# Kernel tuning notes

Hardware: AMD Instinct MI355X
Metric: run time of the kernel (lower is better)

## Reference

```python
import jax, jax.numpy as jnp
import numpy as np
from jax import lax

WINDOW_SIZE = 11
SIGMA = 1.5
DATA_RANGE = 1.0
C1 = (0.01 * DATA_RANGE) ** 2
C2 = (0.03 * DATA_RANGE) ** 2


def _gauss_1d():
    half = WINDOW_SIZE // 2
    xs = np.arange(WINDOW_SIZE, dtype=np.float32)
    g = np.exp(-((xs - half) ** 2) / (2.0 * SIGMA ** 2)).astype(np.float32)
    g = g / g.sum()
    return jnp.asarray(g)


def _blur3d(v, g1d):
    """Depthwise 3D Gaussian blur via three separable 1D convs (same math as
    conv3d with the outer-product window, padding=window_size//2)."""
    C = v.shape[1]
    pad = WINDOW_SIZE // 2
    dn = lax.conv_dimension_numbers(v.shape, (C, 1, WINDOW_SIZE, 1, 1),
                                    ('NCDHW', 'OIDHW', 'NCDHW'))
    for axis in range(3):  # D, H, W
        kshape = [1, 1, 1]
        kshape[axis] = WINDOW_SIZE
        kern = jnp.broadcast_to(g1d.reshape(kshape)[None, None], (C, 1, *kshape))
        padding = [(0, 0)] * 3
        padding[axis] = (pad, pad)
        v = lax.conv_general_dilated(v, kern, window_strides=(1, 1, 1),
                                     padding=padding, dimension_numbers=dn,
                                     feature_group_count=C)
    return v


def setup_inputs() -> dict:
    key = jax.random.key(0)
    k1, k2 = jax.random.split(key)
    shape = (2, 1, 160, 160, 160)
    x = jax.random.uniform(k1, shape, dtype=jnp.float32)
    y = jax.random.uniform(k2, shape, dtype=jnp.float32)
    return {"x": x, "y": y}


def reference(x, y):
    g1d = _gauss_1d()
    mu_x = _blur3d(x, g1d)
    mu_y = _blur3d(y, g1d)
    mu_x_sq = mu_x * mu_x
    mu_y_sq = mu_y * mu_y
    mu_xy = mu_x * mu_y
    sigma_x_sq = _blur3d(x * x, g1d) - mu_x_sq
    sigma_y_sq = _blur3d(y * y, g1d) - mu_y_sq
    sigma_xy = _blur3d(x * y, g1d) - mu_xy
    ssim_map = ((2.0 * mu_xy + C1) * (2.0 * sigma_xy + C2)) / (
        (mu_x_sq + mu_y_sq + C1) * (sigma_x_sq + sigma_y_sq + C2))
    return ssim_map.mean()  # size_average=True
```

## Files before the change

kernel.cpp:

```cpp
#include <hip/hip_runtime.h>
#include <cmath>

#define WS  11
#define NX  160
#define NXY (NX*NX)
#define NB  2
#define TH  16
#define TW  32
#define MH  26
#define MST 36
#define DCHUNK 40
#define PLANE_I 8192000

struct GaussW { float g[WS]; };

__global__ __launch_bounds__(256, 5) void k_wh(const float* __restrict__ x,
                                               const float* __restrict__ y,
                                               float* __restrict__ A,
                                               GaussW gw) {
    __shared__ float mid[5][MH][MST];

    const int tid = threadIdx.x;
    const int b  = blockIdx.z / NX;
    const int d  = blockIdx.z % NX;
    const int h0 = blockIdx.y * TH;
    const int w0 = blockIdx.x * TW;
    const int slice = (b * NX + d) * NXY;

    if (tid < 208) {
        const int wr = tid >> 3;
        const int wq = tid & 7;
        const int gh = h0 - 5 + wr;
        const bool rowok = (unsigned)gh < (unsigned)NX;
        const int c0 = w0 + 4 * wq - 8;
        const int rbase = slice + gh * NX;

        float wx[20], wy[20];
        #pragma unroll
        for (int i = 0; i < 5; ++i) {
            const int ci = c0 + 4 * i;
            float4 xv = {0,0,0,0}, yv = {0,0,0,0};
            if (rowok) {
                if (ci >= 0 && ci + 3 < NX) {
                    xv = *(const float4*)(x + rbase + ci);
                    yv = *(const float4*)(y + rbase + ci);
                } else {
                    float ex[4] = {0,0,0,0}, ey[4] = {0,0,0,0};
                    #pragma unroll
                    for (int e = 0; e < 4; ++e)
                        if ((unsigned)(ci + e) < (unsigned)NX) {
                            ex[e] = x[rbase + ci + e];
                            ey[e] = y[rbase + ci + e];
                        }
                    xv = make_float4(ex[0], ex[1], ex[2], ex[3]);
                    yv = make_float4(ey[0], ey[1], ey[2], ey[3]);
                }
            }
            wx[4*i] = xv.x; wx[4*i+1] = xv.y; wx[4*i+2] = xv.z; wx[4*i+3] = xv.w;
            wy[4*i] = yv.x; wy[4*i+1] = yv.y; wy[4*i+2] = yv.z; wy[4*i+3] = yv.w;
        }
        float a0[4] = {0,0,0,0}, a1[4] = {0,0,0,0}, a2[4] = {0,0,0,0},
              a3[4] = {0,0,0,0}, a4[4] = {0,0,0,0};
        #pragma unroll
        for (int k = 0; k < WS; ++k) {
            const float gk = gw.g[k];
            #pragma unroll
            for (int jj = 0; jj < 4; ++jj) {
                const float xv = wx[3 + jj + k];
                const float yv = wy[3 + jj + k];
                const float t0 = gk * xv, t1 = gk * yv;
                a0[jj] += t0;       a1[jj] += t1;
                a2[jj] += t0 * xv;  a3[jj] += t1 * yv;  a4[jj] += t0 * yv;
            }
        }
        *(float4*)&mid[0][wr][4*wq] = make_float4(a0[0], a0[1], a0[2], a0[3]);
        *(float4*)&mid[1][wr][4*wq] = make_float4(a1[0], a1[1], a1[2], a1[3]);
        *(float4*)&mid[2][wr][4*wq] = make_float4(a2[0], a2[1], a2[2], a2[3]);
        *(float4*)&mid[3][wr][4*wq] = make_float4(a3[0], a3[1], a3[2], a3[3]);
        *(float4*)&mid[4][wr][4*wq] = make_float4(a4[0], a4[1], a4[2], a4[3]);
    }
    __syncthreads();

    if (tid < 160) {
        const int hf  = tid >> 5;
        const int hr0 = ((tid >> 3) & 3) << 2;
        const int hq4 = (tid & 7) << 2;
        float4 o0 = {0,0,0,0}, o1 = {0,0,0,0}, o2 = {0,0,0,0}, o3 = {0,0,0,0};
        #pragma unroll
        for (int k2 = 0; k2 < 14; ++k2) {
            const float4 v = *(const float4*)&mid[hf][hr0 + k2][hq4];
            if (k2 <= 10) { const float g = gw.g[k2];
                o0.x += g*v.x; o0.y += g*v.y; o0.z += g*v.z; o0.w += g*v.w; }
            if (k2 >= 1 && k2 <= 11) { const float g = gw.g[k2-1];
                o1.x += g*v.x; o1.y += g*v.y; o1.z += g*v.z; o1.w += g*v.w; }
            if (k2 >= 2 && k2 <= 12) { const float g = gw.g[k2-2];
                o2.x += g*v.x; o2.y += g*v.y; o2.z += g*v.z; o2.w += g*v.w; }
            if (k2 >= 3) { const float g = gw.g[k2-3];
                o3.x += g*v.x; o3.y += g*v.y; o3.z += g*v.z; o3.w += g*v.w; }
        }
        const int obase = hf * PLANE_I + slice + (h0 + hr0) * NX + w0 + hq4;
        *(float4*)(A + obase)          = o0;
        *(float4*)(A + obase + NX)     = o1;
        *(float4*)(A + obase + 2*NX)   = o2;
        *(float4*)(A + obase + 3*NX)   = o3;
    }
}

__global__ __launch_bounds__(256) void k_d(const float* __restrict__ A,
                                           float* __restrict__ partial,
                                           GaussW gw) {
    const int tid = threadIdx.x;
    const long long gidx = (long long)blockIdx.x * 256 + tid;
    const int NCOL = NB * NX * NX;
    const int chunk = (int)(gidx / NCOL);
    const int col   = (int)(gidx % NCOL);
    const int b  = col / (NX * NX);
    const int hw = col % (NX * NX);
    const int base = b * (NX * NXY) + hw;
    const int d0 = chunk * DCHUNK;

    float win[5][WS];
    #pragma unroll
    for (int i = 0; i < WS; ++i) {
        const int di = d0 - 5 + i;
        const bool ok = (di >= 0 && di < NX);
        const int o = base + (ok ? di : 0) * NXY;
        #pragma unroll
        for (int f = 0; f < 5; ++f)
            win[f][i] = ok ? A[f * PLANE_I + o] : 0.f;
    }

    float acc = 0.f;
    for (int dd = 0; dd < DCHUNK; ++dd) {
        float m[5];
        #pragma unroll
        for (int f = 0; f < 5; ++f) {
            float s = 0.f;
            #pragma unroll
            for (int i = 0; i < WS; ++i) s += gw.g[i] * win[f][i];
            m[f] = s;
        }
        const float mux = m[0], muy = m[1];
        const float mux2 = mux * mux, muy2 = muy * muy, muxy = mux * muy;
        const float sxx = m[2] - mux2, syy = m[3] - muy2, sxy = m[4] - muxy;
        const float num = (2.f * muxy + 1.0e-4f) * (2.f * sxy + 9.0e-4f);
        const float den = (mux2 + muy2 + 1.0e-4f) * (sxx + syy + 9.0e-4f);
        acc += num / den;

        const int dn = d0 + dd + 6;
        const bool ok = (dn < NX);
        const int o = base + (ok ? dn : 0) * NXY;
        #pragma unroll
        for (int f = 0; f < 5; ++f) {
            #pragma unroll
            for (int i = 0; i < WS - 1; ++i) win[f][i] = win[f][i + 1];
            win[f][WS - 1] = ok ? A[f * PLANE_I + o] : 0.f;
        }
    }

    for (int off = 32; off > 0; off >>= 1) acc += __shfl_down(acc, off, 64);
    __shared__ float wsum[4];
    if ((tid & 63) == 0) wsum[tid >> 6] = acc;
    __syncthreads();
    if (tid == 0) partial[blockIdx.x] = wsum[0] + wsum[1] + wsum[2] + wsum[3];
}

__global__ __launch_bounds__(256) void k_red(const float* __restrict__ partial,
                                             int n, float* __restrict__ out) {
    double s = 0.0;
    for (int i = threadIdx.x; i < n; i += 256) s += (double)partial[i];
    __shared__ double sd[256];
    sd[threadIdx.x] = s;
    __syncthreads();
    for (int st = 128; st > 0; st >>= 1) {
        if (threadIdx.x < st) sd[threadIdx.x] += sd[threadIdx.x + st];
        __syncthreads();
    }
    if (threadIdx.x == 0)
        out[0] = (float)(sd[0] / (double)((long long)NB * NX * NXY));
}

extern "C" void kernel_launch(void* const* d_in, const int* in_sizes, int n_in,
                              void* d_out, int out_size, void* d_ws, size_t ws_size,
                              hipStream_t stream) {
    const float* x = (const float*)d_in[0];
    const float* y = (const float*)d_in[1];
    float* A = (float*)d_ws;
    float* partial = (float*)((char*)d_ws + (size_t)5 * PLANE_I * sizeof(float));

    GaussW gw;
    {
        float tmp[WS]; float s = 0.f;
        for (int i = 0; i < WS; ++i) {
            const double e = exp(-(double)((i - 5) * (i - 5)) / 4.5);
            tmp[i] = (float)e; s += tmp[i];
        }
        for (int i = 0; i < WS; ++i) gw.g[i] = tmp[i] / s;
    }

    dim3 g1(NX / TW, NX / TH, NB * NX);
    k_wh<<<g1, 256, 0, stream>>>(x, y, A, gw);

    const int nblk2 = (NB * NX * NX * (NX / DCHUNK)) / 256;
    k_d<<<nblk2, 256, 0, stream>>>(A, partial, gw);

    k_red<<<1, 256, 0, stream>>>(partial, nblk2, (float*)d_out);
}
```

Measured before the change: 116.4 us.

## Double-buffer input slices via async global-to-LDS loads across depth planes per block

The W/H blur kernel now has each block process five consecutive depth slices instead of one. It stages each slice's x and y tile into LDS with global_load_lds while the previous slice is being computed, and clamps addresses so edge zero-padding is applied in registers. The aim is to hide global load latency behind compute and cut per-block launch overhead. In exchange the kernel uses more LDS, lowers the occupancy hint from 5 to 4, and adds extra barriers per slice.

```diff
diff --git a/kernel.cpp b/kernel.cpp
--- a/kernel.cpp
+++ b/kernel.cpp
@@ -9,100 +9,141 @@
 #define TW  32
 #define MH  26
 #define MST 36
+#define SST 48
+#define DPB 5
 #define DCHUNK 40
 #define PLANE_I 8192000
 
 struct GaussW { float g[WS]; };
 
-__global__ __launch_bounds__(256, 5) void k_wh(const float* __restrict__ x,
-                                               const float* __restrict__ y,
-                                               float* __restrict__ A,
-                                               GaussW gw) {
+__device__ __forceinline__ void gload_lds16(const float* g, void* l) {
+    __builtin_amdgcn_global_load_lds(
+        (const __attribute__((address_space(1))) void*)g,
+        (__attribute__((address_space(3))) void*)l, 16, 0, 0);
+}
+
+__global__ __launch_bounds__(256, 4) void k_whp(const float* __restrict__ x,
+                                                const float* __restrict__ y,
+                                                float* __restrict__ A,
+                                                GaussW gw) {
+    __shared__ float sx[2][MH][SST];
+    __shared__ float sy[2][MH][SST];
     __shared__ float mid[5][MH][MST];
 
     const int tid = threadIdx.x;
-    const int b  = blockIdx.z / NX;
-    const int d  = blockIdx.z % NX;
+    const int w0 = blockIdx.x * TW;
     const int h0 = blockIdx.y * TH;
-    const int w0 = blockIdx.x * TW;
-    const int slice = (b * NX + d) * NXY;
-
-    if (tid < 208) {
-        const int wr = tid >> 3;
-        const int wq = tid & 7;
-        const int gh = h0 - 5 + wr;
-        const bool rowok = (unsigned)gh < (unsigned)NX;
-        const int c0 = w0 + 4 * wq - 8;
-        const int rbase = slice + gh * NX;
-
-        float wx[20], wy[20];
-        #pragma unroll
-        for (int i = 0; i < 5; ++i) {
-            const int ci = c0 + 4 * i;
-            float4 xv = {0,0,0,0}, yv = {0,0,0,0};
+    const int b  = blockIdx.z >> 5;
+    const int d0 = (blockIdx.z & 31) * DPB;
+    const int vol = b * (NX * NXY);
+
+    const int r0s = tid / 12, q0s = tid % 12;
+    const int a0g = vol + min(max(h0 - 5 + r0s, 0), NX - 1) * NX
+                        + min(max(w0 - 8 + 4 * q0s, 0), NX - 4);
+    const int ch1 = 256 + tid;
+    const int r1s = ch1 / 12, q1s = ch1 % 12;
+    const int a1g = vol + min(max(h0 - 5 + r1s, 0), NX - 1) * NX
+                        + min(max(w0 - 8 + 4 * q1s, 0), NX - 4);
+    const int wvoff = (tid >> 6) << 10;
+
+    const int wr = tid >> 3;
+    const int wq = tid & 7;
+    const bool wbact = tid < 208;
+    const bool rowok = (unsigned)(h0 - 5 + wr) < (unsigned)NX;
+    const bool edgeblk = (w0 == 0) || (w0 == NX - TW);
+
+    const int hf  = tid >> 5;
+    const int hr0 = ((tid >> 3) & 3) << 2;
+    const int hq4 = (tid & 7) << 2;
+    const bool hbact = tid < 160;
+    const int obase0 = hf * PLANE_I + vol + (h0 + hr0) * NX + w0 + hq4;
+
+    auto stage = [&](int buf, int d) {
+        const int dof = d * NXY;
+        gload_lds16(x + a0g + dof, (char*)&sx[buf][0][0] + wvoff);
+        gload_lds16(y + a0g + dof, (char*)&sy[buf][0][0] + wvoff);
+        if (tid < 56) {
+            gload_lds16(x + a1g + dof, (char*)&sx[buf][0][0] + 4096);
+            gload_lds16(y + a1g + dof, (char*)&sy[buf][0][0] + 4096);
+        }
+    };
+
+    stage(0, d0);
+    __syncthreads();
+
+    int cur = 0;
+    for (int s = 0; s < DPB; ++s) {
+        if (s + 1 < DPB) stage(cur ^ 1, d0 + s + 1);
+
+        if (wbact) {
             if (rowok) {
-                if (ci >= 0 && ci + 3 < NX) {
-                    xv = *(const float4*)(x + rbase + ci);
-                    yv = *(const float4*)(y + rbase + ci);
-                } else {
-                    float ex[4] = {0,0,0,0}, ey[4] = {0,0,0,0};
+                float wx[20], wy[20];
+                #pragma unroll
+                for (int i = 0; i < 5; ++i) {
+                    const float4 xv = *(const float4*)&sx[cur][wr][4 * wq + 4 * i];
+                    const float4 yv = *(const float4*)&sy[cur][wr][4 * wq + 4 * i];
+                    wx[4*i] = xv.x; wx[4*i+1] = xv.y; wx[4*i+2] = xv.z; wx[4*i+3] = xv.w;
+                    wy[4*i] = yv.x; wy[4*i+1] = yv.y; wy[4*i+2] = yv.z; wy[4*i+3] = yv.w;
+                }
+                if (edgeblk) {
                     #pragma unroll
-                    for (int e = 0; e < 4; ++e)
-                        if ((unsigned)(ci + e) < (unsigned)NX) {
-                            ex[e] = x[rbase + ci + e];
-                            ey[e] = y[rbase + ci + e];
+                    for (int m = 0; m < 20; ++m)
+                        if ((unsigned)(w0 - 8 + 4 * wq + m) >= (unsigned)NX) {
+                            wx[m] = 0.f; wy[m] = 0.f;
                         }
-                    xv = make_float4(ex[0], ex[1], ex[2], ex[3]);
-                    yv = make_float4(ey[0], ey[1], ey[2], ey[3]);
                 }
+                float a0[4] = {0,0,0,0}, a1[4] = {0,0,0,0}, a2[4] = {0,0,0,0},
+                      a3[4] = {0,0,0,0}, a4[4] = {0,0,0,0};
+                #pragma unroll
+                for (int k = 0; k < WS; ++k) {
+                    const float gk = gw.g[k];
+                    #pragma unroll
+                    for (int jj = 0; jj < 4; ++jj) {
+                        const float xv = wx[3 + jj + k];
+                        const float yv = wy[3 + jj + k];
+                        const float t0 = gk * xv, t1 = gk * yv;
+                        a0[jj] += t0;       a1[jj] += t1;
+                        a2[jj] += t0 * xv;  a3[jj] += t1 * yv;  a4[jj] += t0 * yv;
+                    }
+                }
+                *(float4*)&mid[0][wr][4*wq] = make_float4(a0[0], a0[1], a0[2], a0[3]);
+                *(float4*)&mid[1][wr][4*wq] = make_float4(a1[0], a1[1], a1[2], a1[3]);
+                *(float4*)&mid[2][wr][4*wq] = make_float4(a2[0], a2[1], a2[2], a2[3]);
+                *(float4*)&mid[3][wr][4*wq] = make_float4(a3[0], a3[1], a3[2], a3[3]);
+                *(float4*)&mid[4][wr][4*wq] = make_float4(a4[0], a4[1], a4[2], a4[3]);
+            } else {
+                const float4 z4 = make_float4(0.f, 0.f, 0.f, 0.f);
+                *(float4*)&mid[0][wr][4*wq] = z4;
+                *(float4*)&mid[1][wr][4*wq] = z4;
+                *(float4*)&mid[2][wr][4*wq] = z4;
+                *(float4*)&mid[3][wr][4*wq] = z4;
+                *(float4*)&mid[4][wr][4*wq] = z4;
             }
-            wx[4*i] = xv.x; wx[4*i+1] = xv.y; wx[4*i+2] = xv.z; wx[4*i+3] = xv.w;
-            wy[4*i] = yv.x; wy[4*i+1] = yv.y; wy[4*i+2] = yv.z; wy[4*i+3] = yv.w;
-        }
-        float a0[4] = {0,0,0,0}, a1[4] = {0,0,0,0}, a2[4] = {0,0,0,0},
-              a3[4] = {0,0,0,0}, a4[4] = {0,0,0,0};
-        #pragma unroll
-        for (int k = 0; k < WS; ++k) {
-            const float gk = gw.g[k];
+        }
+        __syncthreads();
+
+        if (hbact) {
+            float4 o0 = {0,0,0,0}, o1 = {0,0,0,0}, o2 = {0,0,0,0}, o3 = {0,0,0,0};
             #pragma unroll
-            for (int jj = 0; jj < 4; ++jj) {
-                const float xv = wx[3 + jj + k];
-                const float yv = wy[3 + jj + k];
-                const float t0 = gk * xv, t1 = gk * yv;
-                a0[jj] += t0;       a1[jj] += t1;
-                a2[jj] += t0 * xv;  a3[jj] += t1 * yv;  a4[jj] += t0 * yv;
+            for (int k2 = 0; k2 < 14; ++k2) {
+                const float4 v = *(const float4*)&mid[hf][hr0 + k2][hq4];
+                if (k2 <= 10) { const float g = gw.g[k2];
+                    o0.x += g*v.x; o0.y += g*v.y; o0.z += g*v.z; o0.w += g*v.w; }
+                if (k2 >= 1 && k2 <= 11) { const float g = gw.g[k2-1];
+                    o1.x += g*v.x; o1.y += g*v.y; o1.z += g*v.z; o1.w += g*v.w; }
+                if (k2 >= 2 && k2 <= 12) { const float g = gw.g[k2-2];
+                    o2.x += g*v.x; o2.y += g*v.y; o2.z += g*v.z; o2.w += g*v.w; }
+                if (k2 >= 3) { const float g = gw.g[k2-3];
+                    o3.x += g*v.x; o3.y += g*v.y; o3.z += g*v.z; o3.w += g*v.w; }
             }
-        }
-        *(float4*)&mid[0][wr][4*wq] = make_float4(a0[0], a0[1], a0[2], a0[3]);
-        *(float4*)&mid[1][wr][4*wq] = make_float4(a1[0], a1[1], a1[2], a1[3]);
-        *(float4*)&mid[2][wr][4*wq] = make_float4(a2[0], a2[1], a2[2], a2[3]);
-        *(float4*)&mid[3][wr][4*wq] = make_float4(a3[0], a3[1], a3[2], a3[3]);
-        *(float4*)&mid[4][wr][4*wq] = make_float4(a4[0], a4[1], a4[2], a4[3]);
-    }
-    __syncthreads();
-
-    if (tid < 160) {
-        const int hf  = tid >> 5;
-        const int hr0 = ((tid >> 3) & 3) << 2;
-        const int hq4 = (tid & 7) << 2;
-        float4 o0 = {0,0,0,0}, o1 = {0,0,0,0}, o2 = {0,0,0,0}, o3 = {0,0,0,0};
-        #pragma unroll
-        for (int k2 = 0; k2 < 14; ++k2) {
-            const float4 v = *(const float4*)&mid[hf][hr0 + k2][hq4];
-            if (k2 <= 10) { const float g = gw.g[k2];
-                o0.x += g*v.x; o0.y += g*v.y; o0.z += g*v.z; o0.w += g*v.w; }
-            if (k2 >= 1 && k2 <= 11) { const float g = gw.g[k2-1];
-                o1.x += g*v.x; o1.y += g*v.y; o1.z += g*v.z; o1.w += g*v.w; }
-            if (k2 >= 2 && k2 <= 12) { const float g = gw.g[k2-2];
-                o2.x += g*v.x; o2.y += g*v.y; o2.z += g*v.z; o2.w += g*v.w; }
-            if (k2 >= 3) { const float g = gw.g[k2-3];
-                o3.x += g*v.x; o3.y += g*v.y; o3.z += g*v.z; o3.w += g*v.w; }
-        }
-        const int obase = hf * PLANE_I + slice + (h0 + hr0) * NX + w0 + hq4;
-        *(float4*)(A + obase)          = o0;
-        *(float4*)(A + obase + NX)     = o1;
-        *(float4*)(A + obase + 2*NX)   = o2;
-        *(float4*)(A + obase + 3*NX)   = o3;
+            const int ob = obase0 + (d0 + s) * NXY;
+            *(float4*)(A + ob)          = o0;
+            *(float4*)(A + ob + NX)     = o1;
+            *(float4*)(A + ob + 2*NX)   = o2;
+            *(float4*)(A + ob + 3*NX)   = o3;
+        }
+        __syncthreads();
+        cur ^= 1;
     }
 }
 
@@ -198,8 +239,8 @@
         for (int i = 0; i < WS; ++i) gw.g[i] = tmp[i] / s;
     }
 
-    dim3 g1(NX / TW, NX / TH, NB * NX);
-    k_wh<<<g1, 256, 0, stream>>>(x, y, A, gw);
+    dim3 g1(NX / TW, NX / TH, NB * (NX / DPB));
+    k_whp<<<g1, 256, 0, stream>>>(x, y, A, gw);
 
     const int nblk2 = (NB * NX * NX * (NX / DCHUNK)) / 256;
     k_d<<<nblk2, 256, 0, stream>>>(A, partial, gw);
```

Result: no change. 117.8 us (+1.2%).
